# Kernel optimization log

Measured on AMD Instinct MI355X. Metric: run time of the kernel, lower is better.

The kernel has to match this reference:

```python
import jax, jax.numpy as jnp
import numpy as np

N, L, C, S = 4096, 512, 16, 32


def setup_inputs() -> dict:
    key = jax.random.key(0)
    k1, k2, k3, k4 = jax.random.split(key, 4)
    raw = jax.random.normal(k1, (N, L, C), dtype=jnp.float32)
    # valid log-probs: logsumexp along C is slightly < 0
    log_input_probs = jax.nn.log_softmax(raw, axis=-1) - 0.01
    return {
        "log_input_probs": log_input_probs,
        "logit_initial_state_probs": jax.random.normal(k2, (S,), dtype=jnp.float32),
        "logit_transition_probs": jax.random.normal(k3, (S, C, S), dtype=jnp.float32),
        "logit_accepting_state_probs": jax.random.normal(k4, (S,), dtype=jnp.float32),
    }


def reference(log_input_probs, logit_initial_state_probs, logit_transition_probs,
              logit_accepting_state_probs):
    initial_state_probs = jax.nn.softmax(logit_initial_state_probs, axis=0)          # (S,)
    transition_probs = jax.nn.softmax(logit_transition_probs, axis=2)                # (S,C,S)
    accepting_log = jax.nn.log_sigmoid(logit_accepting_state_probs)                  # (S,)
    input_probs = jnp.exp(log_input_probs)                                           # (N,L,C)

    n = log_input_probs.shape[0]
    p0 = jnp.broadcast_to(initial_state_probs[None, :], (n, initial_state_probs.shape[0]))

    def step(p_state, x_t):
        # p_state: (N,S) prev-state probs; x_t: (N,C) symbol probs at step t
        p_new = jnp.einsum('bp,bc,pcn->bn', p_state, x_t, transition_probs)
        return p_new, None

    xs = jnp.swapaxes(input_probs, 0, 1)  # (L,N,C) for scan over time
    p_final, _ = jax.lax.scan(step, p0, xs)

    log_p_state = jnp.log(p_final + 1e-20)                                           # (N,S)
    log_acceptance = jax.nn.logsumexp(log_p_state + accepting_log[None, :], axis=1)  # (N,)
    return log_acceptance[None]  # (1,N)
```

## Files before the change

### kernel.cpp

```cpp
#include <hip/hip_runtime.h>
#include <math.h>

typedef _Float16 f16;
typedef _Float16 f16x2 __attribute__((ext_vector_type(2)));
typedef _Float16 f16x4 __attribute__((ext_vector_type(4)));
typedef _Float16 f16x8 __attribute__((ext_vector_type(8)));
typedef float    f32x4 __attribute__((ext_vector_type(4)));
typedef float    f32x16 __attribute__((ext_vector_type(16)));

#define NB 4096
#define LT 512
#define NC 16
#define NS 32

#define WS_P0     0
#define WS_SIG    128
#define WS_SUMSIG 256
#define WS_FWDT   512
#define WS_BWDT   (512 + 32768)
#define WS_F      (512 + 65536)
#define WS_G      (WS_F + 32*4096*4)

#if __has_builtin(__builtin_amdgcn_exp2f)
#define EXP2F __builtin_amdgcn_exp2f
#else
#define EXP2F exp2f
#endif

__global__ __launch_bounds__(512) void pdfa_prep(const float* __restrict__ tlogit,
                                                 const float* __restrict__ ilogit,
                                                 const float* __restrict__ alogit,
                                                 char* __restrict__ ws) {
    int tid = threadIdx.x;
    f16* fwdT = (f16*)(ws + WS_FWDT);
    f16* bwdT = (f16*)(ws + WS_BWDT);
    int p = tid >> 4, c = tid & 15;
    const float* row = tlogit + p * 512 + c * 32;
    float mx = row[0];
    for (int n = 1; n < 32; ++n) mx = fmaxf(mx, row[n]);
    float s = 0.f;
    for (int n = 0; n < 32; ++n) s += expf(row[n] - mx);
    float inv = 1.f / s;
    int ht = c >> 3, j = c & 7;
    for (int n = 0; n < 32; ++n) {
        float tv = expf(row[n] - mx) * inv;
        fwdT[p * 512 + (32 * ht + n) * 8 + j] = (f16)tv;
        bwdT[n * 512 + (32 * ht + p) * 8 + j] = (f16)tv;
    }
    if (tid < 32) {
        float m0 = ilogit[0];
        for (int n = 1; n < 32; ++n) m0 = fmaxf(m0, ilogit[n]);
        float s0 = 0.f;
        for (int n = 0; n < 32; ++n) s0 += expf(ilogit[n] - m0);
        ((float*)(ws + WS_P0))[tid]  = 256.f * expf(ilogit[tid] - m0) / s0;
        ((float*)(ws + WS_SIG))[tid] = 256.f / (1.f + expf(-alogit[tid]));
    }
    if (tid == 0) {
        float ss = 0.f;
        for (int n = 0; n < 32; ++n) ss += 1.f / (1.f + expf(-alogit[n]));
        *(float*)(ws + WS_SUMSIG) = ss;
    }
}

#define EC(v) ((f16)EXP2F((v) * 1.44269504089f))

#define KS(M, ACC, CIN) { \
    f16 pv_ = pnew[M]; \
    f16x8 pb_ = {pv_, pv_, pv_, pv_, pv_, pv_, pv_, pv_}; \
    f16x8 bf_ = pb_ * xq8; \
    ACC = __builtin_amdgcn_mfma_f32_32x32x16_f16(af[M], bf_, CIN, 0, 0, 0); }

#define STEP(P, XRAW, TNEXT) { \
    f32x16 a0_, a1_; \
    __builtin_amdgcn_s_setprio(1); \
    KS(0, a0_, z) KS(1, a1_, z) \
    KS(2, a0_, a0_) KS(3, a1_, a1_) \
    __builtin_amdgcn_s_setprio(0); \
    f32x16 pf_ = a0_ + a1_; \
    char* wb_ = lds_pw + (P) * 18432; \
    *(f16x4*)(wb_ + 0  + 8*hi) = f16x4{(f16)pf_[0],  (f16)pf_[1],  (f16)pf_[2],  (f16)pf_[3]};  \
    *(f16x4*)(wb_ + 16 + 8*hi) = f16x4{(f16)pf_[4],  (f16)pf_[5],  (f16)pf_[6],  (f16)pf_[7]};  \
    *(f16x4*)(wb_ + 32 + 8*hi) = f16x4{(f16)pf_[8],  (f16)pf_[9],  (f16)pf_[10], (f16)pf_[11]}; \
    *(f16x4*)(wb_ + 48 + 8*hi) = f16x4{(f16)pf_[12], (f16)pf_[13], (f16)pf_[14], (f16)pf_[15]}; \
    *(f16*)(lds_xw + (((P)^1) * 1280)) = EC(XRAW); \
    XRAW = xg[(size_t)(TNEXT) * NC]; \
    __syncthreads(); \
    const char* rb_ = lds_pr + (P) * 18432; \
    f16x4 q0_ = *(const f16x4*)(rb_); \
    f16x4 q1_ = *(const f16x4*)(rb_ + 1 * 2304); \
    f16x4 q2_ = *(const f16x4*)(rb_ + 2 * 2304); \
    f16x4 q3_ = *(const f16x4*)(rb_ + 3 * 2304); \
    f16x4 q4_ = *(const f16x4*)(rb_ + 4 * 2304); \
    f16x4 q5_ = *(const f16x4*)(rb_ + 5 * 2304); \
    f16x4 q6_ = *(const f16x4*)(rb_ + 6 * 2304); \
    f16x4 q7_ = *(const f16x4*)(rb_ + 7 * 2304); \
    xq8 = *(const f16x8*)(lds_xr + (((P)^1) * 1280)); \
    pnew = ((q0_ + q1_) + (q2_ + q3_)) + ((q4_ + q5_) + (q6_ + q7_)); }

__global__ __launch_bounds__(512, 1) void pdfa_main(const float* __restrict__ login,
                                                    char* __restrict__ ws) {
    __shared__ __align__(16) char partb[2 * 18432 + 2 * 1280];
    const int tid  = threadIdx.x;
    const int w    = tid >> 6;
    const int lane = tid & 63;
    const int br   = tid & 31;
    const int hi   = (tid >> 5) & 1;
    const int bid  = blockIdx.x;
    const int dir  = bid & 1;
    const int b0   = (bid >> 1) << 5;

    const char* tblb = ws + (dir ? WS_BWDT : WS_FWDT);
    f16x8 af[4];
#pragma unroll
    for (int m = 0; m < 4; ++m)
        af[m] = *(const f16x8*)(tblb + (4 * w + m) * 1024 + lane * 16);

    const float* initv = (const float*)(ws + (dir ? WS_SIG : WS_P0));
    f16x4 pnew;
#pragma unroll
    for (int j = 0; j < 4; ++j) pnew[j] = (f16)initv[4 * w + j];

    char* lds_pw = &partb[0] + w * 2304 + br * 72;
    const char* lds_pr = &partb[0] + br * 72 + 8 * w;
    char* xbase_lds = &partb[0] + 2 * 18432;
    char* lds_xw = xbase_lds + br * 40 + (8 * hi + w) * 2;
    const char* lds_xr = xbase_lds + br * 40 + hi * 16;

    const float* xg = login + (size_t)(b0 + br) * (LT * NC) + 8 * hi + w;

    const f32x16 z{};
    f16x8 xq8;
    float xrA, xrB;

#define TT(S) (dir ? (511 - (S)) : (S))
    xrA = xg[(size_t)TT(0) * NC];
    xrB = xg[(size_t)TT(1) * NC];
    *(f16*)(lds_xw) = EC(xrA);
    xrA = xg[(size_t)TT(2) * NC];
    __syncthreads();
    xq8 = *(const f16x8*)(lds_xr);

    for (int s = 0; s < 256; s += 2) {
        STEP(0, xrB, TT(s + 3))
        STEP(1, xrA, TT(s + 4))
    }
#undef TT

    if (hi == 0) {
        float* outv = (float*)(ws + (dir ? WS_G : WS_F));
#pragma unroll
        for (int j = 0; j < 4; ++j)
            outv[(size_t)(4 * w + j) * NB + b0 + br] = (float)pnew[j];
    }
}

__global__ __launch_bounds__(256) void pdfa_combine(const char* __restrict__ ws,
                                                    float* __restrict__ out) {
    int b = blockIdx.x * 256 + threadIdx.x;
    const float* f = (const float*)(ws + WS_F);
    const float* g = (const float*)(ws + WS_G);
    float ss = *(const float*)(ws + WS_SUMSIG);
    float dot = 0.f;
#pragma unroll
    for (int s2 = 0; s2 < 32; ++s2)
        dot = fmaf(f[s2 * NB + b], g[s2 * NB + b], dot);
    out[b] = logf(dot * (1.f / 65536.f) + 1e-20f * ss);
}

extern "C" void kernel_launch(void* const* d_in, const int* in_sizes, int n_in,
                              void* d_out, int out_size, void* d_ws, size_t ws_size,
                              hipStream_t stream) {
    const float* login = (const float*)d_in[0];
    const float* ilog  = (const float*)d_in[1];
    const float* tlog  = (const float*)d_in[2];
    const float* alog  = (const float*)d_in[3];
    char* ws = (char*)d_ws;

    pdfa_prep<<<1, 512, 0, stream>>>(tlog, ilog, alog, ws);
    pdfa_main<<<256, 512, 0, stream>>>(login, ws);
    pdfa_combine<<<NB / 256, 256, 0, stream>>>(ws, (float*)d_out);
}
```

Before: 159.5 us.

## Switch recurrence to 16x16x32 MFMA with 16-batch blocks and double grid

Each block now handles 16 sequences instead of 32 and uses 16x16x32 f16 MFMAs in place of 32x32x16. The transition-table layout in the prep kernel and the LDS partial-sum layout are rearranged to match. The grid doubles to 512 blocks, and launch bounds allow several blocks per CU, which spreads the latency-bound serial scan across more CUs and overlaps multiple blocks. Each MFMA is shorter, at the cost of more blocks re-reading tables, and only half the threads now produce x values.

```diff
diff --git a/kernel.cpp b/kernel.cpp
--- a/kernel.cpp
+++ b/kernel.cpp
@@ -6,7 +6,6 @@
 typedef _Float16 f16x4 __attribute__((ext_vector_type(4)));
 typedef _Float16 f16x8 __attribute__((ext_vector_type(8)));
 typedef float    f32x4 __attribute__((ext_vector_type(4)));
-typedef float    f32x16 __attribute__((ext_vector_type(16)));
 
 #define NB 4096
 #define LT 512
@@ -41,11 +40,13 @@
     float s = 0.f;
     for (int n = 0; n < 32; ++n) s += expf(row[n] - mx);
     float inv = 1.f / s;
-    int ht = c >> 3, j = c & 7;
+    int chalf = c >> 3, j = c & 7;
     for (int n = 0; n < 32; ++n) {
         float tv = expf(row[n] - mx) * inv;
-        fwdT[p * 512 + (32 * ht + n) * 8 + j] = (f16)tv;
-        bwdT[n * 512 + (32 * ht + p) * 8 + j] = (f16)tv;
+        fwdT[((((p >> 2) * 2 + ((p >> 1) & 1)) * 2 + (n >> 4)) * 64
+              + 16 * (2 * (p & 1) + chalf) + (n & 15)) * 8 + j] = (f16)tv;
+        bwdT[((((n >> 2) * 2 + ((n >> 1) & 1)) * 2 + (p >> 4)) * 64
+              + 16 * (2 * (n & 1) + chalf) + (p & 15)) * 8 + j] = (f16)tv;
     }
     if (tid < 32) {
         float m0 = ilogit[0];
@@ -64,81 +65,86 @@
 
 #define EC(v) ((f16)EXP2F((v) * 1.44269504089f))
 
-#define KS(M, ACC, CIN) { \
-    f16 pv_ = pnew[M]; \
-    f16x8 pb_ = {pv_, pv_, pv_, pv_, pv_, pv_, pv_, pv_}; \
-    f16x8 bf_ = pb_ * xq8; \
-    ACC = __builtin_amdgcn_mfma_f32_32x32x16_f16(af[M], bf_, CIN, 0, 0, 0); }
+#define XBUF_OFF 16384
 
 #define STEP(P, XRAW, TNEXT) { \
-    f32x16 a0_, a1_; \
+    f16 p0_ = h32 ? pnew[1] : pnew[0]; \
+    f16 p1_ = h32 ? pnew[3] : pnew[2]; \
+    f16x8 pb0_ = {p0_, p0_, p0_, p0_, p0_, p0_, p0_, p0_}; \
+    f16x8 pb1_ = {p1_, p1_, p1_, p1_, p1_, p1_, p1_, p1_}; \
+    f16x8 b0_ = pb0_ * xq8; \
+    f16x8 b1_ = pb1_ * xq8; \
     __builtin_amdgcn_s_setprio(1); \
-    KS(0, a0_, z) KS(1, a1_, z) \
-    KS(2, a0_, a0_) KS(3, a1_, a1_) \
+    f32x4 aR0_ = __builtin_amdgcn_mfma_f32_16x16x32_f16(af[0][0], b0_, z4, 0, 0, 0); \
+    f32x4 aR1_ = __builtin_amdgcn_mfma_f32_16x16x32_f16(af[1][0], b0_, z4, 0, 0, 0); \
+    aR0_ = __builtin_amdgcn_mfma_f32_16x16x32_f16(af[0][1], b1_, aR0_, 0, 0, 0); \
+    aR1_ = __builtin_amdgcn_mfma_f32_16x16x32_f16(af[1][1], b1_, aR1_, 0, 0, 0); \
     __builtin_amdgcn_s_setprio(0); \
-    f32x16 pf_ = a0_ + a1_; \
-    char* wb_ = lds_pw + (P) * 18432; \
-    *(f16x4*)(wb_ + 0  + 8*hi) = f16x4{(f16)pf_[0],  (f16)pf_[1],  (f16)pf_[2],  (f16)pf_[3]};  \
-    *(f16x4*)(wb_ + 16 + 8*hi) = f16x4{(f16)pf_[4],  (f16)pf_[5],  (f16)pf_[6],  (f16)pf_[7]};  \
-    *(f16x4*)(wb_ + 32 + 8*hi) = f16x4{(f16)pf_[8],  (f16)pf_[9],  (f16)pf_[10], (f16)pf_[11]}; \
-    *(f16x4*)(wb_ + 48 + 8*hi) = f16x4{(f16)pf_[12], (f16)pf_[13], (f16)pf_[14], (f16)pf_[15]}; \
-    *(f16*)(lds_xw + (((P)^1) * 1280)) = EC(XRAW); \
-    XRAW = xg[(size_t)(TNEXT) * NC]; \
+    char* wp_ = lds + (P) * 8192 + w * 1024 + lane * 8; \
+    *(f16x4*)(wp_)       = f16x4{(f16)aR0_[0], (f16)aR0_[1], (f16)aR0_[2], (f16)aR0_[3]}; \
+    *(f16x4*)(wp_ + 512) = f16x4{(f16)aR1_[0], (f16)aR1_[1], (f16)aR1_[2], (f16)aR1_[3]}; \
+    if (produce) { \
+        *(f16*)(xw + (((P)^1)) * 768) = EC(XRAW); \
+        XRAW = xg[(size_t)(TNEXT) * NC]; \
+    } \
     __syncthreads(); \
-    const char* rb_ = lds_pr + (P) * 18432; \
-    f16x4 q0_ = *(const f16x4*)(rb_); \
-    f16x4 q1_ = *(const f16x4*)(rb_ + 1 * 2304); \
-    f16x4 q2_ = *(const f16x4*)(rb_ + 2 * 2304); \
-    f16x4 q3_ = *(const f16x4*)(rb_ + 3 * 2304); \
-    f16x4 q4_ = *(const f16x4*)(rb_ + 4 * 2304); \
-    f16x4 q5_ = *(const f16x4*)(rb_ + 5 * 2304); \
-    f16x4 q6_ = *(const f16x4*)(rb_ + 6 * 2304); \
-    f16x4 q7_ = *(const f16x4*)(rb_ + 7 * 2304); \
-    xq8 = *(const f16x8*)(lds_xr + (((P)^1) * 1280)); \
+    const char* rp_ = lds + (P) * 8192 + (w >> 2) * 512 + (w & 3) * 128 + col * 8; \
+    f16x4 q0_ = *(const f16x4*)(rp_); \
+    f16x4 q1_ = *(const f16x4*)(rp_ + 1024); \
+    f16x4 q2_ = *(const f16x4*)(rp_ + 2048); \
+    f16x4 q3_ = *(const f16x4*)(rp_ + 3072); \
+    f16x4 q4_ = *(const f16x4*)(rp_ + 4096); \
+    f16x4 q5_ = *(const f16x4*)(rp_ + 5120); \
+    f16x4 q6_ = *(const f16x4*)(rp_ + 6144); \
+    f16x4 q7_ = *(const f16x4*)(rp_ + 7168); \
+    xq8 = *(const f16x8*)(xr_base + (((P)^1)) * 768); \
     pnew = ((q0_ + q1_) + (q2_ + q3_)) + ((q4_ + q5_) + (q6_ + q7_)); }
 
-__global__ __launch_bounds__(512, 1) void pdfa_main(const float* __restrict__ login,
+__global__ __launch_bounds__(512, 4) void pdfa_main(const float* __restrict__ login,
                                                     char* __restrict__ ws) {
-    __shared__ __align__(16) char partb[2 * 18432 + 2 * 1280];
+    __shared__ __align__(16) char lds[2 * 8192 + 2 * 768];
     const int tid  = threadIdx.x;
     const int w    = tid >> 6;
     const int lane = tid & 63;
-    const int br   = tid & 31;
-    const int hi   = (tid >> 5) & 1;
+    const int col  = lane & 15;
+    const int chalf = (lane >> 4) & 1;
+    const int h32  = lane >> 5;
     const int bid  = blockIdx.x;
     const int dir  = bid & 1;
-    const int b0   = (bid >> 1) << 5;
+    const int b0   = (bid >> 1) << 4;
 
     const char* tblb = ws + (dir ? WS_BWDT : WS_FWDT);
-    f16x8 af[4];
+    f16x8 af[2][2];
 #pragma unroll
-    for (int m = 0; m < 4; ++m)
-        af[m] = *(const f16x8*)(tblb + (4 * w + m) * 1024 + lane * 16);
+    for (int r = 0; r < 2; ++r)
+#pragma unroll
+        for (int kc = 0; kc < 2; ++kc)
+            af[r][kc] = *(const f16x8*)(tblb + (((w * 2 + kc) * 2 + r) * 64 + lane) * 16);
 
     const float* initv = (const float*)(ws + (dir ? WS_SIG : WS_P0));
     f16x4 pnew;
 #pragma unroll
     for (int j = 0; j < 4; ++j) pnew[j] = (f16)initv[4 * w + j];
 
-    char* lds_pw = &partb[0] + w * 2304 + br * 72;
-    const char* lds_pr = &partb[0] + br * 72 + 8 * w;
-    char* xbase_lds = &partb[0] + 2 * 18432;
-    char* lds_xw = xbase_lds + br * 40 + (8 * hi + w) * 2;
-    const char* lds_xr = xbase_lds + br * 40 + hi * 16;
+    const bool produce = (tid < 256);
+    const int colv = (tid >> 4) & 15, cv = tid & 15;
+    const float* xg = login + (size_t)(b0 + colv) * (LT * NC) + cv;
+    char* xw = lds + XBUF_OFF + colv * 48 + (cv >> 3) * 16 + (cv & 7) * 2;
+    const char* xr_base = lds + XBUF_OFF + col * 48 + chalf * 16;
 
-    const float* xg = login + (size_t)(b0 + br) * (LT * NC) + 8 * hi + w;
-
-    const f32x16 z{};
+    const f32x4 z4{};
     f16x8 xq8;
-    float xrA, xrB;
+    float xrA = 0.f, xrB = 0.f;
 
 #define TT(S) (dir ? (511 - (S)) : (S))
-    xrA = xg[(size_t)TT(0) * NC];
-    xrB = xg[(size_t)TT(1) * NC];
-    *(f16*)(lds_xw) = EC(xrA);
-    xrA = xg[(size_t)TT(2) * NC];
+    if (produce) {
+        xrA = xg[(size_t)TT(0) * NC];
+        xrB = xg[(size_t)TT(1) * NC];
+        *(f16*)(xw) = EC(xrA);
+        xrA = xg[(size_t)TT(2) * NC];
+    }
     __syncthreads();
-    xq8 = *(const f16x8*)(lds_xr);
+    xq8 = *(const f16x8*)(xr_base);
 
     for (int s = 0; s < 256; s += 2) {
         STEP(0, xrB, TT(s + 3))
@@ -146,11 +152,11 @@
     }
 #undef TT
 
-    if (hi == 0) {
+    if (lane < 16) {
         float* outv = (float*)(ws + (dir ? WS_G : WS_F));
 #pragma unroll
         for (int j = 0; j < 4; ++j)
-            outv[(size_t)(4 * w + j) * NB + b0 + br] = (float)pnew[j];
+            outv[(size_t)(4 * w + j) * NB + b0 + col] = (float)pnew[j];
     }
 }
 
@@ -177,6 +183,6 @@
     char* ws = (char*)d_ws;
 
     pdfa_prep<<<1, 512, 0, stream>>>(tlog, ilog, alog, ws);
-    pdfa_main<<<256, 512, 0, stream>>>(login, ws);
+    pdfa_main<<<512, 512, 0, stream>>>(login, ws);
     pdfa_combine<<<NB / 256, 256, 0, stream>>>(ws, (float*)d_out);
 }
```

New measurement: 143.4 us, median of 2. 10.1% less time.
